# Kernel optimization log

Measured on AMD Instinct MI355X. Metric: run time of the kernel, lower is better.

Reference implementation:

```python
import jax, jax.numpy as jnp
import numpy as np

NUM_LEVELS = 16
FEATURES_PER_LEVEL = 2
LOG2_HASHMAP_SIZE = 19
HASHMAP_SIZE = 2 ** LOG2_HASHMAP_SIZE
BASE_RES = 16
FINEST_RES = 512
B_GROWTH = np.exp((np.log(FINEST_RES) - np.log(BASE_RES)) / (NUM_LEVELS - 1))
# 8 trilinear corner offsets [8, 3]
OFFSETS = jnp.array([[dx, dy, dz] for dx in (0, 1) for dy in (0, 1) for dz in (0, 1)], dtype=jnp.int32)
PRIMES = jnp.array([1, 73856093, 19349663], dtype=jnp.int32)


def setup_inputs() -> dict:
    key = jax.random.key(0)
    k1, k2 = jax.random.split(key)
    positions = jax.random.uniform(k1, (16, 65536, 3), dtype=jnp.float32, minval=-1.0, maxval=1.0)
    tables = jax.random.normal(k2, (NUM_LEVELS, HASHMAP_SIZE, FEATURES_PER_LEVEL), dtype=jnp.float32) * 0.01
    return {"positions": positions, "tables": tables}


def _encode(positions, tables):
    pos = (positions + 1.0) * 0.5  # [B,S,3] in [0,1]
    outs = []
    for level in range(NUM_LEVELS):
        res = int(np.floor(BASE_RES * B_GROWTH ** level))
        scaled = pos * (res - 1)  # [B,S,3]
        base = jnp.floor(scaled).astype(jnp.int32)
        frac = scaled - base.astype(scaled.dtype)  # [B,S,3]
        corners = base[None] + OFFSETS[:, None, None, :]  # [8,B,S,3]
        # int32 wrapping overflow matches torch's .int() arithmetic; mod gives non-negative
        h = (corners * PRIMES).sum(-1, dtype=jnp.int32) % HASHMAP_SIZE  # [8,B,S]
        feats = tables[level][h]  # [8,B,S,F]
        w = jnp.where(OFFSETS[:, None, None, :] == 1, frac[None], 1.0 - frac[None]).prod(-1)  # [8,B,S]
        outs.append((feats * w[..., None]).sum(0))  # [B,S,F]
    return jnp.concatenate(outs, axis=-1)  # [B,S,L*F]


def reference(positions, tables):
    return _encode(positions, tables)
```

## Files before the change

kernel.cpp:

```cpp
#include <hip/hip_runtime.h>

#define NLEVELS 16
#define HSIZE (1u << 19)
#define HMASK ((1u << 19) - 1u)
#define P2 73856093u
#define P3 19349663u

typedef float nf4 __attribute__((ext_vector_type(4)));
typedef float nf2 __attribute__((ext_vector_type(2)));

__constant__ int c_res[NLEVELS] = {16, 20, 25, 32, 40, 50, 64, 80,
                                   101, 128, 161, 203, 256, 322, 406, 512};

template <bool TO_WS>
__global__ __launch_bounds__(256) void hashgrid_kernel(
    const float* __restrict__ positions,
    const float* __restrict__ tables,
    float2* __restrict__ dst,
    int npoints)
{
    int nch = (npoints + 255) >> 8;
    int b = blockIdx.x;
    int L, chunk;
    if (TO_WS) {
        int xcd = b & 7;
        int j = b >> 3;
        L = xcd + ((j >= nch) ? 8 : 0);
        chunk = (j >= nch) ? (j - nch) : j;
    } else {
        L = b / nch;
        chunk = b - L * nch;
    }
    int p = (chunk << 8) + threadIdx.x;
    if (p >= npoints) return;

    float px = (positions[3 * p + 0] + 1.0f) * 0.5f;
    float py = (positions[3 * p + 1] + 1.0f) * 0.5f;
    float pz = (positions[3 * p + 2] + 1.0f) * 0.5f;

    float rm1 = (float)(c_res[L] - 1);
    float sx = px * rm1, sy = py * rm1, sz = pz * rm1;
    float bx = floorf(sx), by = floorf(sy), bz = floorf(sz);
    float fx = sx - bx, fy = sy - by, fz = sz - bz;

    unsigned ix = (unsigned)(int)bx;
    unsigned iy = (unsigned)(int)by;
    unsigned iz = (unsigned)(int)bz;

    unsigned s00 = ix + iy * P2 + iz * P3;
    unsigned hl0 = s00 & HMASK;
    unsigned hl1 = (s00 + P2) & HMASK;
    unsigned hl2 = (s00 + P3) & HMASK;
    unsigned hl3 = (s00 + P2 + P3) & HMASK;

    const float* tabf = tables + (size_t)L * (2u * HSIZE);
    float2 t0 = ((const float2*)tabf)[0];

    unsigned w0 = (hl0 == HMASK) ? 1u : 0u;
    unsigned w1 = (hl1 == HMASK) ? 1u : 0u;
    unsigned w2 = (hl2 == HMASK) ? 1u : 0u;
    unsigned w3 = (hl3 == HMASK) ? 1u : 0u;

    nf4 g0 = *(const nf4*)(tabf + 2u * (hl0 - w0));
    nf4 g1 = *(const nf4*)(tabf + 2u * (hl1 - w1));
    nf4 g2 = *(const nf4*)(tabf + 2u * (hl2 - w2));
    nf4 g3 = *(const nf4*)(tabf + 2u * (hl3 - w3));

    float l0x = w0 ? g0.z : g0.x, l0y = w0 ? g0.w : g0.y;
    float h0x = w0 ? t0.x : g0.z, h0y = w0 ? t0.y : g0.w;
    float l1x = w1 ? g1.z : g1.x, l1y = w1 ? g1.w : g1.y;
    float h1x = w1 ? t0.x : g1.z, h1y = w1 ? t0.y : g1.w;
    float l2x = w2 ? g2.z : g2.x, l2y = w2 ? g2.w : g2.y;
    float h2x = w2 ? t0.x : g2.z, h2y = w2 ? t0.y : g2.w;
    float l3x = w3 ? g3.z : g3.x, l3y = w3 ? g3.w : g3.y;
    float h3x = w3 ? t0.x : g3.z, h3y = w3 ? t0.y : g3.w;

    float wx0 = 1.0f - fx, wy0 = 1.0f - fy, wz0 = 1.0f - fz;
    float c0 = wy0 * wz0;
    float c1 = fy * wz0;
    float c2 = wy0 * fz;
    float c3 = fy * fz;

    float o0 = c0 * (wx0 * l0x + fx * h0x)
             + c1 * (wx0 * l1x + fx * h1x)
             + c2 * (wx0 * l2x + fx * h2x)
             + c3 * (wx0 * l3x + fx * h3x);
    float o1 = c0 * (wx0 * l0y + fx * h0y)
             + c1 * (wx0 * l1y + fx * h1y)
             + c2 * (wx0 * l2y + fx * h2y)
             + c3 * (wx0 * l3y + fx * h3y);

    if (TO_WS) {
        nf2 v = {o0, o1};
        __builtin_nontemporal_store(
            v, (nf2*)dst + ((size_t)chunk * NLEVELS + L) * 256 + threadIdx.x);
    } else {
        dst[(size_t)p * NLEVELS + L] = make_float2(o0, o1);
    }
}

__global__ __launch_bounds__(256) void transpose_kernel(
    const nf4* __restrict__ ws4,
    nf4* __restrict__ out4,
    int npoints)
{
    __shared__ float2 lds[256][NLEVELS + 1];
    int c = blockIdx.x;
    int t = threadIdx.x;
    size_t base = (size_t)c * 2048;

#pragma unroll
    for (int k = 0; k < 8; ++k) {
        int i = (k << 8) + t;
        nf4 v = __builtin_nontemporal_load(&ws4[base + i]);
        int L = i >> 7;
        int m = i & 127;
        lds[m][L]       = make_float2(v.x, v.y);
        lds[m + 128][L] = make_float2(v.z, v.w);
    }
    __syncthreads();

#pragma unroll
    for (int k = 0; k < 8; ++k) {
        int i = (k << 8) + t;
        int pp = i >> 3;
        int q = i & 7;
        int r = (pp >> 1) | ((pp & 1) << 7);
        float2 a = lds[r][2 * q];
        float2 bb = lds[r][2 * q + 1];
        nf4 v = {a.x, a.y, bb.x, bb.y};
        __builtin_nontemporal_store(v, &out4[base + i]);
    }
}

extern "C" void kernel_launch(void* const* d_in, const int* in_sizes, int n_in,
                              void* d_out, int out_size, void* d_ws, size_t ws_size,
                              hipStream_t stream) {
    const float* positions = (const float*)d_in[0];
    const float* tables = (const float*)d_in[1];
    int npoints = in_sizes[0] / 3;
    int nch = (npoints + 255) >> 8;
    int blocks = NLEVELS * nch;

    size_t ws_needed = (size_t)NLEVELS * npoints * sizeof(float2);
    if (ws_size >= ws_needed && (npoints & 255) == 0) {
        float2* ws = (float2*)d_ws;
        hashgrid_kernel<true><<<blocks, 256, 0, stream>>>(positions, tables, ws, npoints);
        transpose_kernel<<<npoints / 256, 256, 0, stream>>>((const nf4*)ws,
                                                            (nf4*)d_out, npoints);
    } else {
        hashgrid_kernel<false><<<blocks, 256, 0, stream>>>(positions, tables,
                                                           (float2*)d_out, npoints);
    }
}
```

Baseline: 509.4 us.

## Process two points per thread and batch eight gathers before use

```diff
diff --git a/kernel.cpp b/kernel.cpp
--- a/kernel.cpp
+++ b/kernel.cpp
@@ -19,7 +19,7 @@
     float2* __restrict__ dst,
     int npoints)
 {
-    int nch = (npoints + 255) >> 8;
+    int nch = (npoints + 511) >> 9;
     int b = blockIdx.x;
     int L, chunk;
     if (TO_WS) {
@@ -31,71 +31,98 @@
         L = b / nch;
         chunk = b - L * nch;
     }
-    int p = (chunk << 8) + threadIdx.x;
-    if (p >= npoints) return;
+    int t = threadIdx.x;
+    int p0 = (chunk << 9) + (t << 1);
+    if (p0 >= npoints) return;
+    bool haveB = (p0 + 1 < npoints);
 
-    float px = (positions[3 * p + 0] + 1.0f) * 0.5f;
-    float py = (positions[3 * p + 1] + 1.0f) * 0.5f;
-    float pz = (positions[3 * p + 2] + 1.0f) * 0.5f;
+    const float2* pos2 = (const float2*)positions + ((size_t)chunk * 768 + 3 * t);
+    float2 f01 = pos2[0];
+    float2 f23 = pos2[1];
+    float2 f45 = haveB ? pos2[2] : make_float2(f01.x, f01.y);
+
+    float pAx = (f01.x + 1.0f) * 0.5f, pAy = (f01.y + 1.0f) * 0.5f, pAz = (f23.x + 1.0f) * 0.5f;
+    float pBx = (f23.y + 1.0f) * 0.5f, pBy = (f45.x + 1.0f) * 0.5f, pBz = (f45.y + 1.0f) * 0.5f;
+    if (!haveB) { pBx = pAx; pBy = pAy; pBz = pAz; }
 
     float rm1 = (float)(c_res[L] - 1);
-    float sx = px * rm1, sy = py * rm1, sz = pz * rm1;
-    float bx = floorf(sx), by = floorf(sy), bz = floorf(sz);
-    float fx = sx - bx, fy = sy - by, fz = sz - bz;
 
-    unsigned ix = (unsigned)(int)bx;
-    unsigned iy = (unsigned)(int)by;
-    unsigned iz = (unsigned)(int)bz;
+    float sAx = pAx * rm1, sAy = pAy * rm1, sAz = pAz * rm1;
+    float bAx = floorf(sAx), bAy = floorf(sAy), bAz = floorf(sAz);
+    float fAx = sAx - bAx, fAy = sAy - bAy, fAz = sAz - bAz;
+    unsigned sA = (unsigned)(int)bAx + (unsigned)(int)bAy * P2 + (unsigned)(int)bAz * P3;
+    unsigned hA0 = sA & HMASK,             hA1 = (sA + P2) & HMASK;
+    unsigned hA2 = (sA + P3) & HMASK,      hA3 = (sA + P2 + P3) & HMASK;
 
-    unsigned s00 = ix + iy * P2 + iz * P3;
-    unsigned hl0 = s00 & HMASK;
-    unsigned hl1 = (s00 + P2) & HMASK;
-    unsigned hl2 = (s00 + P3) & HMASK;
-    unsigned hl3 = (s00 + P2 + P3) & HMASK;
+    float sBx = pBx * rm1, sBy = pBy * rm1, sBz = pBz * rm1;
+    float bBx = floorf(sBx), bBy = floorf(sBy), bBz = floorf(sBz);
+    float fBx = sBx - bBx, fBy = sBy - bBy, fBz = sBz - bBz;
+    unsigned sB = (unsigned)(int)bBx + (unsigned)(int)bBy * P2 + (unsigned)(int)bBz * P3;
+    unsigned hB0 = sB & HMASK,             hB1 = (sB + P2) & HMASK;
+    unsigned hB2 = (sB + P3) & HMASK,      hB3 = (sB + P2 + P3) & HMASK;
 
     const float* tabf = tables + (size_t)L * (2u * HSIZE);
+
+    unsigned wA0 = (hA0 == HMASK) ? 1u : 0u, wA1 = (hA1 == HMASK) ? 1u : 0u;
+    unsigned wA2 = (hA2 == HMASK) ? 1u : 0u, wA3 = (hA3 == HMASK) ? 1u : 0u;
+    unsigned wB0 = (hB0 == HMASK) ? 1u : 0u, wB1 = (hB1 == HMASK) ? 1u : 0u;
+    unsigned wB2 = (hB2 == HMASK) ? 1u : 0u, wB3 = (hB3 == HMASK) ? 1u : 0u;
+
+    nf4 g0 = *(const nf4*)(tabf + 2u * (hA0 - wA0));
+    nf4 g1 = *(const nf4*)(tabf + 2u * (hA1 - wA1));
+    nf4 g2 = *(const nf4*)(tabf + 2u * (hA2 - wA2));
+    nf4 g3 = *(const nf4*)(tabf + 2u * (hA3 - wA3));
+    nf4 g4 = *(const nf4*)(tabf + 2u * (hB0 - wB0));
+    nf4 g5 = *(const nf4*)(tabf + 2u * (hB1 - wB1));
+    nf4 g6 = *(const nf4*)(tabf + 2u * (hB2 - wB2));
+    nf4 g7 = *(const nf4*)(tabf + 2u * (hB3 - wB3));
+    asm volatile("" :: "v"(g0), "v"(g1), "v"(g2), "v"(g3),
+                       "v"(g4), "v"(g5), "v"(g6), "v"(g7));
+
     float2 t0 = ((const float2*)tabf)[0];
 
-    unsigned w0 = (hl0 == HMASK) ? 1u : 0u;
-    unsigned w1 = (hl1 == HMASK) ? 1u : 0u;
-    unsigned w2 = (hl2 == HMASK) ? 1u : 0u;
-    unsigned w3 = (hl3 == HMASK) ? 1u : 0u;
+    float lx, ly, hx, hy;
+    float wx0, wy0, wz0, c0, c1, c2, c3;
 
-    nf4 g0 = *(const nf4*)(tabf + 2u * (hl0 - w0));
-    nf4 g1 = *(const nf4*)(tabf + 2u * (hl1 - w1));
-    nf4 g2 = *(const nf4*)(tabf + 2u * (hl2 - w2));
-    nf4 g3 = *(const nf4*)(tabf + 2u * (hl3 - w3));
+    wx0 = 1.0f - fAx; wy0 = 1.0f - fAy; wz0 = 1.0f - fAz;
+    c0 = wy0 * wz0; c1 = fAy * wz0; c2 = wy0 * fAz; c3 = fAy * fAz;
+    float oA0 = 0.0f, oA1 = 0.0f;
+    lx = wA0 ? g0.z : g0.x; ly = wA0 ? g0.w : g0.y;
+    hx = wA0 ? t0.x : g0.z; hy = wA0 ? t0.y : g0.w;
+    oA0 += c0 * (wx0 * lx + fAx * hx); oA1 += c0 * (wx0 * ly + fAx * hy);
+    lx = wA1 ? g1.z : g1.x; ly = wA1 ? g1.w : g1.y;
+    hx = wA1 ? t0.x : g1.z; hy = wA1 ? t0.y : g1.w;
+    oA0 += c1 * (wx0 * lx + fAx * hx); oA1 += c1 * (wx0 * ly + fAx * hy);
+    lx = wA2 ? g2.z : g2.x; ly = wA2 ? g2.w : g2.y;
+    hx = wA2 ? t0.x : g2.z; hy = wA2 ? t0.y : g2.w;
+    oA0 += c2 * (wx0 * lx + fAx * hx); oA1 += c2 * (wx0 * ly + fAx * hy);
+    lx = wA3 ? g3.z : g3.x; ly = wA3 ? g3.w : g3.y;
+    hx = wA3 ? t0.x : g3.z; hy = wA3 ? t0.y : g3.w;
+    oA0 += c3 * (wx0 * lx + fAx * hx); oA1 += c3 * (wx0 * ly + fAx * hy);
 
-    float l0x = w0 ? g0.z : g0.x, l0y = w0 ? g0.w : g0.y;
-    float h0x = w0 ? t0.x : g0.z, h0y = w0 ? t0.y : g0.w;
-    float l1x = w1 ? g1.z : g1.x, l1y = w1 ? g1.w : g1.y;
-    float h1x = w1 ? t0.x : g1.z, h1y = w1 ? t0.y : g1.w;
-    float l2x = w2 ? g2.z : g2.x, l2y = w2 ? g2.w : g2.y;
-    float h2x = w2 ? t0.x : g2.z, h2y = w2 ? t0.y : g2.w;
-    float l3x = w3 ? g3.z : g3.x, l3y = w3 ? g3.w : g3.y;
-    float h3x = w3 ? t0.x : g3.z, h3y = w3 ? t0.y : g3.w;
-
-    float wx0 = 1.0f - fx, wy0 = 1.0f - fy, wz0 = 1.0f - fz;
-    float c0 = wy0 * wz0;
-    float c1 = fy * wz0;
-    float c2 = wy0 * fz;
-    float c3 = fy * fz;
-
-    float o0 = c0 * (wx0 * l0x + fx * h0x)
-             + c1 * (wx0 * l1x + fx * h1x)
-             + c2 * (wx0 * l2x + fx * h2x)
-             + c3 * (wx0 * l3x + fx * h3x);
-    float o1 = c0 * (wx0 * l0y + fx * h0y)
-             + c1 * (wx0 * l1y + fx * h1y)
-             + c2 * (wx0 * l2y + fx * h2y)
-             + c3 * (wx0 * l3y + fx * h3y);
+    wx0 = 1.0f - fBx; wy0 = 1.0f - fBy; wz0 = 1.0f - fBz;
+    c0 = wy0 * wz0; c1 = fBy * wz0; c2 = wy0 * fBz; c3 = fBy * fBz;
+    float oB0 = 0.0f, oB1 = 0.0f;
+    lx = wB0 ? g4.z : g4.x; ly = wB0 ? g4.w : g4.y;
+    hx = wB0 ? t0.x : g4.z; hy = wB0 ? t0.y : g4.w;
+    oB0 += c0 * (wx0 * lx + fBx * hx); oB1 += c0 * (wx0 * ly + fBx * hy);
+    lx = wB1 ? g5.z : g5.x; ly = wB1 ? g5.w : g5.y;
+    hx = wB1 ? t0.x : g5.z; hy = wB1 ? t0.y : g5.w;
+    oB0 += c1 * (wx0 * lx + fBx * hx); oB1 += c1 * (wx0 * ly + fBx * hy);
+    lx = wB2 ? g6.z : g6.x; ly = wB2 ? g6.w : g6.y;
+    hx = wB2 ? t0.x : g6.z; hy = wB2 ? t0.y : g6.w;
+    oB0 += c2 * (wx0 * lx + fBx * hx); oB1 += c2 * (wx0 * ly + fBx * hy);
+    lx = wB3 ? g7.z : g7.x; ly = wB3 ? g7.w : g7.y;
+    hx = wB3 ? t0.x : g7.z; hy = wB3 ? t0.y : g7.w;
+    oB0 += c3 * (wx0 * lx + fBx * hx); oB1 += c3 * (wx0 * ly + fBx * hy);
 
     if (TO_WS) {
-        nf2 v = {o0, o1};
+        nf4 v = {oA0, oA1, oB0, oB1};
         __builtin_nontemporal_store(
-            v, (nf2*)dst + ((size_t)chunk * NLEVELS + L) * 256 + threadIdx.x);
+            v, (nf4*)dst + ((size_t)chunk * NLEVELS + L) * 256 + t);
     } else {
-        dst[(size_t)p * NLEVELS + L] = make_float2(o0, o1);
+        dst[(size_t)p0 * NLEVELS + L] = make_float2(oA0, oA1);
+        if (haveB) dst[(size_t)(p0 + 1) * NLEVELS + L] = make_float2(oB0, oB1);
     }
 }
 
@@ -105,21 +132,34 @@
     int npoints)
 {
     __shared__ float2 lds[256][NLEVELS + 1];
-    int c = blockIdx.x;
+    int cb = blockIdx.x;
     int t = threadIdx.x;
-    size_t base = (size_t)c * 2048;
+    int chunk = cb >> 1, h = cb & 1;
+    size_t hb = (size_t)chunk * 4096 + (size_t)h * 128;
 
+    nf4 v0 = __builtin_nontemporal_load(&ws4[hb + ((0 * 256 + t) >> 7) * 256 + ((0 * 256 + t) & 127)]);
+    nf4 v1 = __builtin_nontemporal_load(&ws4[hb + ((1 * 256 + t) >> 7) * 256 + ((1 * 256 + t) & 127)]);
+    nf4 v2 = __builtin_nontemporal_load(&ws4[hb + ((2 * 256 + t) >> 7) * 256 + ((2 * 256 + t) & 127)]);
+    nf4 v3 = __builtin_nontemporal_load(&ws4[hb + ((3 * 256 + t) >> 7) * 256 + ((3 * 256 + t) & 127)]);
+    nf4 v4 = __builtin_nontemporal_load(&ws4[hb + ((4 * 256 + t) >> 7) * 256 + ((4 * 256 + t) & 127)]);
+    nf4 v5 = __builtin_nontemporal_load(&ws4[hb + ((5 * 256 + t) >> 7) * 256 + ((5 * 256 + t) & 127)]);
+    nf4 v6 = __builtin_nontemporal_load(&ws4[hb + ((6 * 256 + t) >> 7) * 256 + ((6 * 256 + t) & 127)]);
+    nf4 v7 = __builtin_nontemporal_load(&ws4[hb + ((7 * 256 + t) >> 7) * 256 + ((7 * 256 + t) & 127)]);
+    asm volatile("" :: "v"(v0), "v"(v1), "v"(v2), "v"(v3),
+                       "v"(v4), "v"(v5), "v"(v6), "v"(v7));
+
+    nf4 vv[8] = {v0, v1, v2, v3, v4, v5, v6, v7};
 #pragma unroll
     for (int k = 0; k < 8; ++k) {
         int i = (k << 8) + t;
-        nf4 v = __builtin_nontemporal_load(&ws4[base + i]);
         int L = i >> 7;
         int m = i & 127;
-        lds[m][L]       = make_float2(v.x, v.y);
-        lds[m + 128][L] = make_float2(v.z, v.w);
+        lds[m][L]       = make_float2(vv[k].x, vv[k].y);
+        lds[m + 128][L] = make_float2(vv[k].z, vv[k].w);
     }
     __syncthreads();
 
+    size_t base = (size_t)cb * 2048;
 #pragma unroll
     for (int k = 0; k < 8; ++k) {
         int i = (k << 8) + t;
@@ -139,11 +179,11 @@
     const float* positions = (const float*)d_in[0];
     const float* tables = (const float*)d_in[1];
     int npoints = in_sizes[0] / 3;
-    int nch = (npoints + 255) >> 8;
+    int nch = (npoints + 511) >> 9;
     int blocks = NLEVELS * nch;
 
     size_t ws_needed = (size_t)NLEVELS * npoints * sizeof(float2);
-    if (ws_size >= ws_needed && (npoints & 255) == 0) {
+    if (ws_size >= ws_needed && (npoints & 511) == 0) {
         float2* ws = (float2*)d_ws;
         hashgrid_kernel<true><<<blocks, 256, 0, stream>>>(positions, tables, ws, npoints);
         transpose_kernel<<<npoints / 256, 256, 0, stream>>>((const nf4*)ws,
```

Result: slower. 524.0 us (+2.9%).
